# Optimization experiments

Hardware: AMD Instinct MI355X
Metric: run time of the kernel (lower is better)

## Reference

```python
import jax, jax.numpy as jnp
import numpy as np

def setup_inputs() -> dict:
    key = jax.random.key(0)
    inputs_embeds = jax.random.normal(key, (16, 8192, 256), dtype=jnp.float32)
    return {"inputs_embeds": inputs_embeds}

def reference(inputs_embeds):
    # cumulative prefix mean along seq dim: mean over [:i+1] = cumsum / (i+1)
    S = inputs_embeds.shape[1]
    csum = jnp.cumsum(inputs_embeds, axis=1)  # [B, S, D]
    denom = jnp.arange(1, S + 1, dtype=inputs_embeds.dtype)[None, :, None]
    return (csum / denom,)
```

## Files before the change

kernel.cpp:

```cpp
#include <hip/hip_runtime.h>

#define BB 16
#define SS 8192
#define DD 256
#define NC 64
#define CL (SS / NC)

__global__ __launch_bounds__(256) void avgseq_chunksum(const float* __restrict__ x,
                                                       float* __restrict__ ws) {
    const int blk = blockIdx.x;
    const int b = blk / NC;
    const int c = blk % NC;
    const int d = threadIdx.x;

    const float* p = x + ((size_t)b * SS + (size_t)c * CL) * DD + d;
    float acc = 0.0f;
#pragma unroll 8
    for (int s = 0; s < CL; ++s) {
        acc += p[(size_t)s * DD];
    }
    ws[((size_t)b * NC + c) * DD + d] = acc;
}

__global__ __launch_bounds__(256) void avgseq_scan(const float* __restrict__ x,
                                                   const float* __restrict__ ws,
                                                   float* __restrict__ out) {
    const int blk = blockIdx.x;
    const int b = blk / NC;
    const int c = blk % NC;
    const int d = threadIdx.x;

    const float* w = ws + (size_t)b * NC * DD + d;
    float prefix = 0.0f;
    for (int cc = 0; cc < c; ++cc) {
        prefix += w[(size_t)cc * DD];
    }

    const size_t base = ((size_t)b * SS + (size_t)c * CL) * DD + d;
    const float* p = x + base;
    float* o = out + base;
    const int s0 = c * CL;

    float acc = prefix;
#pragma unroll 4
    for (int s = 0; s < CL; ++s) {
        acc += p[(size_t)s * DD];
        o[(size_t)s * DD] = acc / (float)(s0 + s + 1);
    }
}

extern "C" void kernel_launch(void* const* d_in, const int* in_sizes, int n_in,
                              void* d_out, int out_size, void* d_ws, size_t ws_size,
                              hipStream_t stream) {
    const float* x = (const float*)d_in[0];
    float* out = (float*)d_out;
    float* ws = (float*)d_ws;

    const int nblocks = BB * NC;
    avgseq_chunksum<<<nblocks, DD, 0, stream>>>(x, ws);
    avgseq_scan<<<nblocks, DD, 0, stream>>>(x, ws, out);
}
```

Baseline: 260.0 us.

## Vectorize chunked prefix-mean scan with float4 and double chunk count

Result: no change. 259.2 us (-0.3%).

```diff
diff --git a/kernel.cpp b/kernel.cpp
--- a/kernel.cpp
+++ b/kernel.cpp
@@ -3,60 +3,67 @@
 #define BB 16
 #define SS 8192
 #define DD 256
-#define NC 64
+#define D4 (DD / 4)
+#define NC 128
 #define CL (SS / NC)
 
-__global__ __launch_bounds__(256) void avgseq_chunksum(const float* __restrict__ x,
-                                                       float* __restrict__ ws) {
+__global__ __launch_bounds__(64) void avgseq_chunksum(const float4* __restrict__ x,
+                                                      float4* __restrict__ ws) {
     const int blk = blockIdx.x;
-    const int b = blk / NC;
-    const int c = blk % NC;
-    const int d = threadIdx.x;
+    const int b = blk >> 7;
+    const int c = blk & (NC - 1);
+    const int t = threadIdx.x;
 
-    const float* p = x + ((size_t)b * SS + (size_t)c * CL) * DD + d;
-    float acc = 0.0f;
+    const float4* p = x + ((size_t)b * SS + (size_t)c * CL) * D4 + t;
+    float4 acc = make_float4(0.f, 0.f, 0.f, 0.f);
 #pragma unroll 8
     for (int s = 0; s < CL; ++s) {
-        acc += p[(size_t)s * DD];
+        float4 v = p[(size_t)s * D4];
+        acc.x += v.x; acc.y += v.y; acc.z += v.z; acc.w += v.w;
     }
-    ws[((size_t)b * NC + c) * DD + d] = acc;
+    ws[((size_t)b * NC + c) * D4 + t] = acc;
 }
 
-__global__ __launch_bounds__(256) void avgseq_scan(const float* __restrict__ x,
-                                                   const float* __restrict__ ws,
-                                                   float* __restrict__ out) {
+__global__ __launch_bounds__(64) void avgseq_scan(const float4* __restrict__ x,
+                                                  const float4* __restrict__ ws,
+                                                  float4* __restrict__ out) {
     const int blk = blockIdx.x;
-    const int b = blk / NC;
-    const int c = blk % NC;
-    const int d = threadIdx.x;
+    const int b = blk >> 7;
+    const int c = blk & (NC - 1);
+    const int t = threadIdx.x;
 
-    const float* w = ws + (size_t)b * NC * DD + d;
-    float prefix = 0.0f;
+    const float4* w = ws + (size_t)b * NC * D4 + t;
+    float4 pre = make_float4(0.f, 0.f, 0.f, 0.f);
+#pragma unroll 4
     for (int cc = 0; cc < c; ++cc) {
-        prefix += w[(size_t)cc * DD];
+        float4 v = w[(size_t)cc * D4];
+        pre.x += v.x; pre.y += v.y; pre.z += v.z; pre.w += v.w;
     }
 
-    const size_t base = ((size_t)b * SS + (size_t)c * CL) * DD + d;
-    const float* p = x + base;
-    float* o = out + base;
+    const size_t base = ((size_t)b * SS + (size_t)c * CL) * D4 + t;
+    const float4* p = x + base;
+    float4* o = out + base;
     const int s0 = c * CL;
 
-    float acc = prefix;
-#pragma unroll 4
+    float4 acc = pre;
+#pragma unroll 8
     for (int s = 0; s < CL; ++s) {
-        acc += p[(size_t)s * DD];
-        o[(size_t)s * DD] = acc / (float)(s0 + s + 1);
+        float4 v = p[(size_t)s * D4];
+        acc.x += v.x; acc.y += v.y; acc.z += v.z; acc.w += v.w;
+        const float r = __builtin_amdgcn_rcpf((float)(s0 + s + 1));
+        float4 ov = make_float4(acc.x * r, acc.y * r, acc.z * r, acc.w * r);
+        o[(size_t)s * D4] = ov;
     }
 }
 
 extern "C" void kernel_launch(void* const* d_in, const int* in_sizes, int n_in,
                               void* d_out, int out_size, void* d_ws, size_t ws_size,
                               hipStream_t stream) {
-    const float* x = (const float*)d_in[0];
-    float* out = (float*)d_out;
-    float* ws = (float*)d_ws;
+    const float4* x = (const float4*)d_in[0];
+    float4* out = (float4*)d_out;
+    float4* ws = (float4*)d_ws;
 
     const int nblocks = BB * NC;
-    avgseq_chunksum<<<nblocks, DD, 0, stream>>>(x, ws);
-    avgseq_scan<<<nblocks, DD, 0, stream>>>(x, ws, out);
+    avgseq_chunksum<<<nblocks, 64, 0, stream>>>(x, ws);
+    avgseq_scan<<<nblocks, 64, 0, stream>>>(x, ws, out);
 }
```

## Fuse chunk-sum and scan into single-pass decoupled scan with float4 loads

Applied to the files above, without the earlier changes.

Result: slower. 540.9 us (+108.1%).

```diff
diff --git a/kernel.cpp b/kernel.cpp
--- a/kernel.cpp
+++ b/kernel.cpp
@@ -3,60 +3,115 @@
 #define BB 16
 #define SS 8192
 #define DD 256
-#define NC 64
-#define CL (SS / NC)
+#define D4 64
+#define NC 128
+#define CL 64
+#define RPT 16
+#define NB (BB * NC)
 
-__global__ __launch_bounds__(256) void avgseq_chunksum(const float* __restrict__ x,
-                                                       float* __restrict__ ws) {
+#define AGG_OFF 4096
+
+__global__ __launch_bounds__(256) void avgseq_onepass(
+    const float4* __restrict__ x, float4* __restrict__ out,
+    unsigned long long* __restrict__ masks, float4* __restrict__ agg)
+{
     const int blk = blockIdx.x;
-    const int b = blk / NC;
-    const int c = blk % NC;
-    const int d = threadIdx.x;
+    const int b   = blk >> 7;
+    const int c   = blk & (NC - 1);
+    const int tid = threadIdx.x;
+    const int col = tid & 63;
+    const int q   = tid >> 6;
 
-    const float* p = x + ((size_t)b * SS + (size_t)c * CL) * DD + d;
-    float acc = 0.0f;
-#pragma unroll 8
-    for (int s = 0; s < CL; ++s) {
-        acc += p[(size_t)s * DD];
+    __shared__ float4 part[4][D4];
+    __shared__ float4 pref[D4];
+
+    const size_t rowbase = ((size_t)b * SS + (size_t)c * CL + (size_t)q * RPT) * D4 + col;
+    const float4* p = x + rowbase;
+
+    float4 v[RPT];
+#pragma unroll
+    for (int i = 0; i < RPT; ++i) v[i] = p[(size_t)i * D4];
+
+    float4 ps = make_float4(0.f, 0.f, 0.f, 0.f);
+#pragma unroll
+    for (int i = 0; i < RPT; ++i) {
+        ps.x += v[i].x; ps.y += v[i].y; ps.z += v[i].z; ps.w += v[i].w;
     }
-    ws[((size_t)b * NC + c) * DD + d] = acc;
-}
+    part[q][col] = ps;
+    __syncthreads();
 
-__global__ __launch_bounds__(256) void avgseq_scan(const float* __restrict__ x,
-                                                   const float* __restrict__ ws,
-                                                   float* __restrict__ out) {
-    const int blk = blockIdx.x;
-    const int b = blk / NC;
-    const int c = blk % NC;
-    const int d = threadIdx.x;
+    if (q == 0) {
+        float4 s0 = part[0][col], s1 = part[1][col], s2 = part[2][col], s3 = part[3][col];
+        float4 cs = make_float4(s0.x + s1.x + s2.x + s3.x,
+                                s0.y + s1.y + s2.y + s3.y,
+                                s0.z + s1.z + s2.z + s3.z,
+                                s0.w + s1.w + s2.w + s3.w);
+        agg[(size_t)blk * D4 + col] = cs;
+        __threadfence();
+        if (col == 0) {
+            __hip_atomic_fetch_or(&masks[b * 2 + (c >> 6)], 1ull << (c & 63),
+                                  __ATOMIC_RELEASE, __HIP_MEMORY_SCOPE_AGENT);
+        }
+        float4 run = make_float4(0.f, 0.f, 0.f, 0.f);
+        if (c > 0) {
+            const unsigned long long need0 =
+                (c >= 64) ? ~0ull : ((1ull << c) - 1ull);
+            const unsigned long long need1 =
+                (c > 64) ? ((1ull << (c - 64)) - 1ull) : 0ull;
+            for (;;) {
+                unsigned long long m0 = __hip_atomic_load(&masks[b * 2 + 0],
+                                       __ATOMIC_ACQUIRE, __HIP_MEMORY_SCOPE_AGENT);
+                unsigned long long m1 = __hip_atomic_load(&masks[b * 2 + 1],
+                                       __ATOMIC_ACQUIRE, __HIP_MEMORY_SCOPE_AGENT);
+                if (((m0 & need0) == need0) && ((m1 & need1) == need1)) break;
+                __builtin_amdgcn_s_sleep(2);
+            }
+            const float4* ap = agg + (size_t)(b * NC) * D4 + col;
+            int cc = 0;
+            for (; cc + 4 <= c; cc += 4) {
+                float4 a0 = ap[(size_t)(cc + 0) * D4];
+                float4 a1 = ap[(size_t)(cc + 1) * D4];
+                float4 a2 = ap[(size_t)(cc + 2) * D4];
+                float4 a3 = ap[(size_t)(cc + 3) * D4];
+                run.x += (a0.x + a1.x) + (a2.x + a3.x);
+                run.y += (a0.y + a1.y) + (a2.y + a3.y);
+                run.z += (a0.z + a1.z) + (a2.z + a3.z);
+                run.w += (a0.w + a1.w) + (a2.w + a3.w);
+            }
+            for (; cc < c; ++cc) {
+                float4 a = ap[(size_t)cc * D4];
+                run.x += a.x; run.y += a.y; run.z += a.z; run.w += a.w;
+            }
+        }
+        pref[col] = run;
+    }
+    __syncthreads();
 
-    const float* w = ws + (size_t)b * NC * DD + d;
-    float prefix = 0.0f;
-    for (int cc = 0; cc < c; ++cc) {
-        prefix += w[(size_t)cc * DD];
+    float4 start = pref[col];
+    for (int qq = 0; qq < q; ++qq) {
+        float4 t = part[qq][col];
+        start.x += t.x; start.y += t.y; start.z += t.z; start.w += t.w;
     }
 
-    const size_t base = ((size_t)b * SS + (size_t)c * CL) * DD + d;
-    const float* p = x + base;
-    float* o = out + base;
-    const int s0 = c * CL;
-
-    float acc = prefix;
-#pragma unroll 4
-    for (int s = 0; s < CL; ++s) {
-        acc += p[(size_t)s * DD];
-        o[(size_t)s * DD] = acc / (float)(s0 + s + 1);
+    const int sg0 = c * CL + q * RPT;
+    float4* o = out + rowbase;
+#pragma unroll
+    for (int i = 0; i < RPT; ++i) {
+        start.x += v[i].x; start.y += v[i].y; start.z += v[i].z; start.w += v[i].w;
+        const float r = __builtin_amdgcn_rcpf((float)(sg0 + i + 1));
+        o[(size_t)i * D4] = make_float4(start.x * r, start.y * r,
+                                        start.z * r, start.w * r);
     }
 }
 
 extern "C" void kernel_launch(void* const* d_in, const int* in_sizes, int n_in,
                               void* d_out, int out_size, void* d_ws, size_t ws_size,
                               hipStream_t stream) {
-    const float* x = (const float*)d_in[0];
-    float* out = (float*)d_out;
-    float* ws = (float*)d_ws;
+    const float4* x = (const float4*)d_in[0];
+    float4* out = (float4*)d_out;
+    unsigned long long* masks = (unsigned long long*)d_ws;
+    float4* agg = (float4*)((char*)d_ws + AGG_OFF);
 
-    const int nblocks = BB * NC;
-    avgseq_chunksum<<<nblocks, DD, 0, stream>>>(x, ws);
-    avgseq_scan<<<nblocks, DD, 0, stream>>>(x, ws, out);
+    hipMemsetAsync(d_ws, 0, AGG_OFF, stream);
+    avgseq_onepass<<<NB, 256, 0, stream>>>(x, out, masks, agg);
 }
```
